# Performance work log

Hardware: AMD Instinct MI355X
Metric: run time of the kernel (lower is better)

The kernel has to match this reference:

```python
import jax, jax.numpy as jnp
import numpy as np

LN_EPS = 1e-5


def setup_inputs() -> dict:
    key = jax.random.key(0)
    kA, kX, kh = jax.random.split(key, 3)
    B, N, Cin, C, K = 16, 1024, 64, 64, 3
    A = jax.random.normal(kA, (B, N, N), dtype=jnp.float32)
    X = jax.random.normal(kX, (B, N, Cin), dtype=jnp.float32)
    h = jax.random.normal(kh, (K + 1, C, N), dtype=jnp.float32)
    ln_gamma = jnp.ones((C,), dtype=jnp.float32)
    ln_beta = jnp.zeros((C,), dtype=jnp.float32)
    return {"A": A, "X": X, "h": h, "ln_gamma": ln_gamma, "ln_beta": ln_beta}


def reference(A, X, h, ln_gamma, ln_beta):
    # Original loops compute, for each output channel c:
    #   sum_i sum_ch diag(h[i,c]) @ A^i @ X[..., ch]
    # which equals sum_i h[i,c,:] * (A^i @ X.sum(-1)).
    num_terms = h.shape[0] - 1  # static
    Xs = X.sum(-1)  # [B, N]
    powers = [Xs]
    p = Xs
    for _ in range(num_terms):  # static small loop over polynomial terms
        p = jnp.einsum('bnm,bm->bn', A, p)  # A^i @ Xs, matrix-vector per batch
        powers.append(p)
    P = jnp.stack(powers)  # [K+1, B, N]
    # node-variant per-channel taps: Y[b,n,c] = sum_i h[i,c,n] * P[i,b,n]
    Y = jnp.einsum('icn,ibn->bnc', h, P)  # [B, N, C]
    mu = Y.mean(axis=-1, keepdims=True)
    var = Y.var(axis=-1, keepdims=True)
    Yn = (Y - mu) / jnp.sqrt(var + LN_EPS) * ln_gamma + ln_beta
    return jnp.tanh(Yn)
```

## Files before the change

### kernel.cpp

```cpp
#include <hip/hip_runtime.h>
#include <math.h>

constexpr int B = 16, N = 1024, Cin = 64, C = 64, K = 3;
constexpr int BN = B * N;
constexpr int GRID = 512;
constexpr int ROWS = 32;
#define LN_EPS 1e-5f

__device__ __forceinline__ void bbar(unsigned int* cnt) {
    __syncthreads();
    if (threadIdx.x == 0) {
        __hip_atomic_fetch_add(cnt, 1u, __ATOMIC_RELAXED, __HIP_MEMORY_SCOPE_AGENT);
        int spins = 0;
        while (__hip_atomic_load(cnt, __ATOMIC_RELAXED, __HIP_MEMORY_SCOPE_AGENT) < 32u) {
            __builtin_amdgcn_s_sleep(8);
            if (++spins > (1 << 17)) break;
        }
    }
    __syncthreads();
}

__global__ void __launch_bounds__(256, 2)
fused_persist(const float* __restrict__ A, const float* __restrict__ X,
              const float* __restrict__ h, const float* __restrict__ gamma,
              const float* __restrict__ beta, float* __restrict__ out,
              unsigned int* __restrict__ bar, float* __restrict__ P) {
    __shared__ __align__(16) union SU {
        float As[16][1024];
        float hl[K + 1][ROWS][65];
    } u;
    __shared__ __align__(16) float4 xs[N / 4];
    __shared__ float p3s[ROWS];
    const int tid   = threadIdx.x;
    const int lane  = tid & 63;
    const int w     = tid >> 6;
    const int b     = blockIdx.x >> 5;
    const int rbase = (blockIdx.x & 31) * ROWS;
    unsigned int* mybar = bar + (size_t)b * 3 * 32;
    const float* Ab = A + ((size_t)b << 20);

    float4 Ar[4][4];
    #pragma unroll
    for (int j = 0; j < 4; ++j) {
        const float4* rp = (const float4*)(Ab + (size_t)(rbase + 16 + w * 4 + j) * N);
        #pragma unroll
        for (int k = 0; k < 4; ++k)
            Ar[j][k] = rp[k * 64 + lane];
    }
    #pragma unroll
    for (int j = 0; j < 4; ++j)
        #pragma unroll
        for (int k = 0; k < 4; ++k)
            asm volatile("" : "+v"(Ar[j][k].x), "+v"(Ar[j][k].y),
                              "+v"(Ar[j][k].z), "+v"(Ar[j][k].w));

    #pragma unroll
    for (int i = 0; i < 16; ++i) {
        int idx  = i * 256 + tid;
        int row  = idx >> 8;
        int col4 = idx & 255;
        ((float4*)u.As[row])[col4] =
            ((const float4*)(Ab + (size_t)(rbase + row) * N))[col4];
    }

    {
        const float* Xb = X + ((size_t)b * N + rbase) * Cin;
        float* P0 = P + (size_t)b * N;
        #pragma unroll
        for (int j = 0; j < 8; ++j) {
            int nn = w * 8 + j;
            float v = Xb[(size_t)nn * Cin + lane];
            #pragma unroll
            for (int off = 32; off; off >>= 1) v += __shfl_xor(v, off);
            if (lane == 0)
                __hip_atomic_store(&P0[rbase + nn], v, __ATOMIC_RELAXED,
                                   __HIP_MEMORY_SCOPE_AGENT);
        }
    }
    bbar(mybar);

    for (int it = 0; it < 3; ++it) {
        const float* xsrc = P + (size_t)it * BN + (size_t)b * N;
        xs[tid] = ((const float4*)xsrc)[tid];
        __syncthreads();

        float accL[4] = {0.f, 0.f, 0.f, 0.f};
        float accR[4] = {0.f, 0.f, 0.f, 0.f};
        #pragma unroll
        for (int k = 0; k < 4; ++k) {
            float4 xx = xs[k * 64 + lane];
            #pragma unroll
            for (int j = 0; j < 4; ++j) {
                float4 aL = ((const float4*)u.As[w * 4 + j])[k * 64 + lane];
                accL[j] += aL.x * xx.x + aL.y * xx.y + aL.z * xx.z + aL.w * xx.w;
                float4 aR = Ar[j][k];
                accR[j] += aR.x * xx.x + aR.y * xx.y + aR.z * xx.z + aR.w * xx.w;
            }
        }
        #pragma unroll
        for (int off = 32; off; off >>= 1)
            #pragma unroll
            for (int j = 0; j < 4; ++j) {
                accL[j] += __shfl_xor(accL[j], off);
                accR[j] += __shfl_xor(accR[j], off);
            }

        if (lane == 0) {
            if (it < 2) {
                float* ydst = P + (size_t)(it + 1) * BN + (size_t)b * N + rbase;
                #pragma unroll
                for (int j = 0; j < 4; ++j) {
                    __hip_atomic_store(&ydst[w * 4 + j],      accL[j],
                                       __ATOMIC_RELAXED, __HIP_MEMORY_SCOPE_AGENT);
                    __hip_atomic_store(&ydst[16 + w * 4 + j], accR[j],
                                       __ATOMIC_RELAXED, __HIP_MEMORY_SCOPE_AGENT);
                }
            } else {
                #pragma unroll
                for (int j = 0; j < 4; ++j) {
                    p3s[w * 4 + j]      = accL[j];
                    p3s[16 + w * 4 + j] = accR[j];
                }
            }
        }
        if (it < 2) bbar(mybar + (1 + it) * 32);
        else        __syncthreads();
    }

    {
        const int i4    = tid >> 6;
        const int cofs  = (tid & 63) >> 3;
        const int nngrp = tid & 7;
        #pragma unroll
        for (int c0 = 0; c0 < 64; c0 += 8) {
            int c = c0 + cofs;
            float4 v = *(const float4*)(h + ((size_t)i4 * C + c) * N + rbase + nngrp * 4);
            int nn0 = nngrp * 4;
            u.hl[i4][nn0 + 0][c] = v.x;
            u.hl[i4][nn0 + 1][c] = v.y;
            u.hl[i4][nn0 + 2][c] = v.z;
            u.hl[i4][nn0 + 3][c] = v.w;
        }
    }
    __syncthreads();

    const float g  = gamma[lane];
    const float be = beta[lane];
    #pragma unroll
    for (int j = 0; j < 8; ++j) {
        const int nn = w * 8 + j;
        const int n  = rbase + nn;
        float y = p3s[nn] * u.hl[3][nn][lane];
        #pragma unroll
        for (int i = 0; i < 3; ++i) {
            float pv = P[(size_t)i * BN + (size_t)b * N + n];
            y += pv * u.hl[i][nn][lane];
        }
        float s = y;
        #pragma unroll
        for (int off = 32; off; off >>= 1) s += __shfl_xor(s, off);
        float mu = s * (1.0f / 64.0f);
        float d  = y - mu;
        float v  = d * d;
        #pragma unroll
        for (int off = 32; off; off >>= 1) v += __shfl_xor(v, off);
        float var = v * (1.0f / 64.0f);
        float yn  = d * rsqrtf(var + LN_EPS) * g + be;
        out[((size_t)b * N + n) * C + lane] = tanhf(yn);
    }
}

extern "C" void kernel_launch(void* const* d_in, const int* in_sizes, int n_in,
                              void* d_out, int out_size, void* d_ws, size_t ws_size,
                              hipStream_t stream) {
    const float* A     = (const float*)d_in[0];
    const float* X     = (const float*)d_in[1];
    const float* h     = (const float*)d_in[2];
    const float* gamma = (const float*)d_in[3];
    const float* beta  = (const float*)d_in[4];
    float* out = (float*)d_out;

    unsigned int* bar = (unsigned int*)d_ws;
    float* P = (float*)((char*)d_ws + 8192);

    hipMemsetAsync(bar, 0, B * 3 * 32 * sizeof(unsigned int), stream);
    fused_persist<<<GRID, 256, 0, stream>>>(A, X, h, gamma, beta, out, bar, P);
}
```

Before: 119.9 us.

## Double block size, use direct global-to-LDS loads, and prefetch h before barrier

Raises the block to 512 threads (8 waves), so each wave handles half as many A rows in registers and shared memory. The shared-memory half of A is now loaded with global_load_lds async copies instead of going through registers. The h taps are loaded into registers before the first grid barrier so their latency hides behind the power iterations. The cost is more VGPR pressure from holding hv, and the occupancy target in launch bounds becomes 4 blocks per CU, which may not fit given the shared-memory footprint.

```diff
diff --git a/kernel.cpp b/kernel.cpp
--- a/kernel.cpp
+++ b/kernel.cpp
@@ -4,6 +4,7 @@
 constexpr int B = 16, N = 1024, Cin = 64, C = 64, K = 3;
 constexpr int BN = B * N;
 constexpr int GRID = 512;
+constexpr int BLOCK = 512;
 constexpr int ROWS = 32;
 #define LN_EPS 1e-5f
 
@@ -20,7 +21,7 @@
     __syncthreads();
 }
 
-__global__ void __launch_bounds__(256, 2)
+__global__ void __launch_bounds__(BLOCK, 4)
 fused_persist(const float* __restrict__ A, const float* __restrict__ X,
               const float* __restrict__ h, const float* __restrict__ gamma,
               const float* __restrict__ beta, float* __restrict__ out,
@@ -39,59 +40,84 @@
     unsigned int* mybar = bar + (size_t)b * 3 * 32;
     const float* Ab = A + ((size_t)b << 20);
 
-    float4 Ar[4][4];
-    #pragma unroll
-    for (int j = 0; j < 4; ++j) {
-        const float4* rp = (const float4*)(Ab + (size_t)(rbase + 16 + w * 4 + j) * N);
+    float xv[4];
+    {
+        const float* Xb = X + ((size_t)b * N + rbase) * Cin;
+        #pragma unroll
+        for (int j = 0; j < 4; ++j)
+            xv[j] = Xb[(size_t)(w * 4 + j) * Cin + lane];
+    }
+
+    #pragma unroll
+    for (int i = 0; i < 8; ++i) {
+        const int wavebase = i * 512 + w * 64;
+        const int row      = wavebase >> 8;
+        const int col4     = (wavebase & 255) + lane;
+        const float* gsrc  = Ab + (size_t)(rbase + row) * N + (size_t)col4 * 4;
+        float* ldst = (float*)(((float4*)&u.As[0][0]) + wavebase);
+        __builtin_amdgcn_global_load_lds(
+            (const __attribute__((address_space(1))) void*)gsrc,
+            (__attribute__((address_space(3))) void*)ldst, 16, 0, 0);
+    }
+
+    float4 Ar[2][4];
+    #pragma unroll
+    for (int j = 0; j < 2; ++j) {
+        const float4* rp = (const float4*)(Ab + (size_t)(rbase + 16 + w * 2 + j) * N);
         #pragma unroll
         for (int k = 0; k < 4; ++k)
             Ar[j][k] = rp[k * 64 + lane];
     }
-    #pragma unroll
-    for (int j = 0; j < 4; ++j)
+
+    const int i4    = tid >> 7;
+    const int cofs  = (tid & 127) >> 3;
+    const int nngrp = tid & 7;
+    float4 hv[4];
+    #pragma unroll
+    for (int c0 = 0; c0 < 4; ++c0) {
+        const int c = c0 * 16 + cofs;
+        hv[c0] = *(const float4*)(h + ((size_t)i4 * C + c) * N + rbase + nngrp * 4);
+    }
+
+    {
+        float* P0 = P + (size_t)b * N;
+        #pragma unroll
+        for (int j = 0; j < 4; ++j) {
+            float v = xv[j];
+            #pragma unroll
+            for (int off = 32; off; off >>= 1) v += __shfl_xor(v, off);
+            if (lane == 0)
+                __hip_atomic_store(&P0[rbase + w * 4 + j], v, __ATOMIC_RELAXED,
+                                   __HIP_MEMORY_SCOPE_AGENT);
+        }
+    }
+
+    #pragma unroll
+    for (int j = 0; j < 2; ++j)
         #pragma unroll
         for (int k = 0; k < 4; ++k)
             asm volatile("" : "+v"(Ar[j][k].x), "+v"(Ar[j][k].y),
                               "+v"(Ar[j][k].z), "+v"(Ar[j][k].w));
-
-    #pragma unroll
-    for (int i = 0; i < 16; ++i) {
-        int idx  = i * 256 + tid;
-        int row  = idx >> 8;
-        int col4 = idx & 255;
-        ((float4*)u.As[row])[col4] =
-            ((const float4*)(Ab + (size_t)(rbase + row) * N))[col4];
-    }
-
-    {
-        const float* Xb = X + ((size_t)b * N + rbase) * Cin;
-        float* P0 = P + (size_t)b * N;
-        #pragma unroll
-        for (int j = 0; j < 8; ++j) {
-            int nn = w * 8 + j;
-            float v = Xb[(size_t)nn * Cin + lane];
-            #pragma unroll
-            for (int off = 32; off; off >>= 1) v += __shfl_xor(v, off);
-            if (lane == 0)
-                __hip_atomic_store(&P0[rbase + nn], v, __ATOMIC_RELAXED,
-                                   __HIP_MEMORY_SCOPE_AGENT);
-        }
-    }
+    #pragma unroll
+    for (int c0 = 0; c0 < 4; ++c0)
+        asm volatile("" : "+v"(hv[c0].x), "+v"(hv[c0].y),
+                          "+v"(hv[c0].z), "+v"(hv[c0].w));
+
     bbar(mybar);
 
     for (int it = 0; it < 3; ++it) {
         const float* xsrc = P + (size_t)it * BN + (size_t)b * N;
-        xs[tid] = ((const float4*)xsrc)[tid];
+        if (tid < 256) xs[tid] = ((const float4*)xsrc)[tid];
         __syncthreads();
 
-        float accL[4] = {0.f, 0.f, 0.f, 0.f};
-        float accR[4] = {0.f, 0.f, 0.f, 0.f};
+        float accL[2] = {0.f, 0.f};
+        float accR[2] = {0.f, 0.f};
         #pragma unroll
         for (int k = 0; k < 4; ++k) {
             float4 xx = xs[k * 64 + lane];
             #pragma unroll
-            for (int j = 0; j < 4; ++j) {
-                float4 aL = ((const float4*)u.As[w * 4 + j])[k * 64 + lane];
+            for (int j = 0; j < 2; ++j) {
+                float4 aL = ((const float4*)u.As[w * 2 + j])[k * 64 + lane];
                 accL[j] += aL.x * xx.x + aL.y * xx.y + aL.z * xx.z + aL.w * xx.w;
                 float4 aR = Ar[j][k];
                 accR[j] += aR.x * xx.x + aR.y * xx.y + aR.z * xx.z + aR.w * xx.w;
@@ -100,7 +126,7 @@
         #pragma unroll
         for (int off = 32; off; off >>= 1)
             #pragma unroll
-            for (int j = 0; j < 4; ++j) {
+            for (int j = 0; j < 2; ++j) {
                 accL[j] += __shfl_xor(accL[j], off);
                 accR[j] += __shfl_xor(accR[j], off);
             }
@@ -109,17 +135,17 @@
             if (it < 2) {
                 float* ydst = P + (size_t)(it + 1) * BN + (size_t)b * N + rbase;
                 #pragma unroll
-                for (int j = 0; j < 4; ++j) {
-                    __hip_atomic_store(&ydst[w * 4 + j],      accL[j],
+                for (int j = 0; j < 2; ++j) {
+                    __hip_atomic_store(&ydst[w * 2 + j],      accL[j],
                                        __ATOMIC_RELAXED, __HIP_MEMORY_SCOPE_AGENT);
-                    __hip_atomic_store(&ydst[16 + w * 4 + j], accR[j],
+                    __hip_atomic_store(&ydst[16 + w * 2 + j], accR[j],
                                        __ATOMIC_RELAXED, __HIP_MEMORY_SCOPE_AGENT);
                 }
             } else {
                 #pragma unroll
-                for (int j = 0; j < 4; ++j) {
-                    p3s[w * 4 + j]      = accL[j];
-                    p3s[16 + w * 4 + j] = accR[j];
+                for (int j = 0; j < 2; ++j) {
+                    p3s[w * 2 + j]      = accL[j];
+                    p3s[16 + w * 2 + j] = accR[j];
                 }
             }
         }
@@ -127,28 +153,22 @@
         else        __syncthreads();
     }
 
-    {
-        const int i4    = tid >> 6;
-        const int cofs  = (tid & 63) >> 3;
-        const int nngrp = tid & 7;
-        #pragma unroll
-        for (int c0 = 0; c0 < 64; c0 += 8) {
-            int c = c0 + cofs;
-            float4 v = *(const float4*)(h + ((size_t)i4 * C + c) * N + rbase + nngrp * 4);
-            int nn0 = nngrp * 4;
-            u.hl[i4][nn0 + 0][c] = v.x;
-            u.hl[i4][nn0 + 1][c] = v.y;
-            u.hl[i4][nn0 + 2][c] = v.z;
-            u.hl[i4][nn0 + 3][c] = v.w;
-        }
+    #pragma unroll
+    for (int c0 = 0; c0 < 4; ++c0) {
+        const int c   = c0 * 16 + cofs;
+        const int nn0 = nngrp * 4;
+        u.hl[i4][nn0 + 0][c] = hv[c0].x;
+        u.hl[i4][nn0 + 1][c] = hv[c0].y;
+        u.hl[i4][nn0 + 2][c] = hv[c0].z;
+        u.hl[i4][nn0 + 3][c] = hv[c0].w;
     }
     __syncthreads();
 
     const float g  = gamma[lane];
     const float be = beta[lane];
     #pragma unroll
-    for (int j = 0; j < 8; ++j) {
-        const int nn = w * 8 + j;
+    for (int j = 0; j < 4; ++j) {
+        const int nn = w * 4 + j;
         const int n  = rbase + nn;
         float y = p3s[nn] * u.hl[3][nn][lane];
         #pragma unroll
@@ -184,5 +204,5 @@
     float* P = (float*)((char*)d_ws + 8192);
 
     hipMemsetAsync(bar, 0, B * 3 * 32 * sizeof(unsigned int), stream);
-    fused_persist<<<GRID, 256, 0, stream>>>(A, X, h, gamma, beta, out, bar, P);
+    fused_persist<<<GRID, BLOCK, 0, stream>>>(A, X, h, gamma, beta, out, bar, P);
 }
```

New measurement: 116.8 us. 2.5% less time.
